# Kernel optimization log

Measured on AMD Instinct MI355X. Metric: run time of the kernel, lower is better.

The kernel has to match this reference:

```python
import jax, jax.numpy as jnp
import numpy as np

N = 100000        # nodes
E = 3200000       # edges (avg degree 32)
IN, HID, OUT = 512, 256, 64
K = 10
ALPHA = 0.1


def setup_inputs() -> dict:
    key = jax.random.key(0)
    k1, k2, k3, k4 = jax.random.split(key, 4)
    x = jax.random.normal(k1, (N, IN), dtype=jnp.float32)
    edge_index = jax.random.randint(k2, (2, E), 0, N, dtype=jnp.int64)
    W1 = jax.random.normal(k3, (IN, HID), dtype=jnp.float32) * (1.0 / np.sqrt(IN))
    b1 = jnp.zeros((HID,), dtype=jnp.float32)
    W2 = jax.random.normal(k4, (HID, OUT), dtype=jnp.float32) * (1.0 / np.sqrt(HID))
    b2 = jnp.zeros((OUT,), dtype=jnp.float32)
    return {"x": x, "edge_index": edge_index, "W1": W1, "b1": b1, "W2": W2, "b2": b2}


def reference(x, edge_index, W1, b1, W2, b2):
    # MLP head: Linear -> ReLU -> Linear
    h = jax.nn.relu(x @ W1 + b1)
    h = h @ W2 + b2                                   # [N, OUT]

    # gcn_norm with self-loops: D^-1/2 (A + I) D^-1/2
    src = jnp.concatenate([edge_index[0], jnp.arange(N, dtype=edge_index.dtype)])
    dst = jnp.concatenate([edge_index[1], jnp.arange(N, dtype=edge_index.dtype)])
    deg = jax.ops.segment_sum(jnp.ones_like(src, dtype=h.dtype), dst, num_segments=N)
    dinv = jnp.where(deg > 0, jax.lax.rsqrt(deg), 0.0)
    norm = dinv[src] * dinv[dst]                      # [E+N]

    h0 = h

    def step(h, _):
        msg = h[src] * norm[:, None]                  # gather + edge scale
        agg = jax.ops.segment_sum(msg, dst, num_segments=N)  # scatter-add
        h = (1.0 - ALPHA) * agg + ALPHA * h0          # teleport
        return h, None

    h, _ = jax.lax.scan(step, h, None, length=K)
    return h
```

## Files before the change

### kernel.cpp

```cpp
#include <hip/hip_runtime.h>
#include <hip/hip_bf16.h>
#include <hip/hip_fp16.h>


typedef __bf16 bf16x8 __attribute__((ext_vector_type(8)));
typedef float f32x4 __attribute__((ext_vector_type(4)));

static constexpr int IN = 512, HID = 256, OUT = 64;
static constexpr int LDT = 40;

static __device__ __forceinline__ ushort f2bf(float f) {
  __hip_bfloat16 b = __float2bfloat16(f);
  return *reinterpret_cast<ushort*>(&b);
}
static __device__ __forceinline__ float bf2f(ushort u) {
  unsigned int x = ((unsigned int)u) << 16;
  return __uint_as_float(x);
}
static __device__ __forceinline__ float h15f(unsigned int u) {
  ushort hb = (ushort)(u & 0x7FFFu);
  __half h = *reinterpret_cast<__half*>(&hb);
  return __half2float(h);
}

static __device__ __forceinline__ void gload16(const void* g, void* l) {
  __builtin_amdgcn_global_load_lds(
      (const __attribute__((address_space(1))) void*)g,
      (__attribute__((address_space(3))) void*)l, 16, 0, 0);
}

__global__ void transpose_f32_bf16(const float* __restrict__ in, ushort* __restrict__ out,
                                   int K, int C) {
  int idx = blockIdx.x * 256 + threadIdx.x;
  if (idx < K * C) {
    int n = idx / K, k = idx % K;
    out[idx] = f2bf(in[k * C + n]);
  }
}

__global__ __launch_bounds__(256) void gemm1(const float* __restrict__ X,
                                             const ushort* __restrict__ W1T,
                                             const float* __restrict__ b1,
                                             ushort* __restrict__ h1, int M) {
  __shared__ __align__(16) float As[2][128 * 32];
  __shared__ __align__(16) ushort Bs[2][128 * 32];
  const int tid = threadIdx.x;
  const int m0 = blockIdx.y * 128;
  const int n0 = blockIdx.x * 128;
  const int lane = tid & 63, w = tid >> 6;
  const int wr = w >> 1, wc = w & 1;
  const int lm = lane & 15, lq = lane >> 4;
  const int wbase = w * 64;

  auto STAGE = [&](int k0, int buf) {
#pragma unroll
    for (int i = 0; i < 4; ++i) {
      int idx = i * 256 + tid;
      int row = idx >> 3, ch = idx & 7;
      int gm = m0 + row; gm = gm < M ? gm : M - 1;
      int sch = ch ^ (row & 7);
      gload16(&X[(size_t)gm * IN + k0 + sch * 4], &As[buf][(i * 256 + wbase) * 4]);
    }
#pragma unroll
    for (int i = 0; i < 2; ++i) {
      int idx = i * 256 + tid;
      int row = idx >> 2, ch = idx & 3;
      int sch = ch ^ ((row ^ (row >> 2)) & 3);
      gload16(&W1T[(size_t)(n0 + row) * IN + k0 + sch * 8], &Bs[buf][(i * 256 + wbase) * 8]);
    }
  };

  f32x4 acc[4][4] = {};

  STAGE(0, 0);
  __syncthreads();

  int cur = 0;
  for (int k0 = 0; k0 < IN; k0 += 32) {
    if (k0 + 32 < IN) STAGE(k0 + 32, cur ^ 1);

    bf16x8 af[4], bq[4];
#pragma unroll
    for (int mi = 0; mi < 4; ++mi) {
      int r = wr * 64 + mi * 16 + lm;
      int k7 = r & 7;
      float4 x0 = *reinterpret_cast<const float4*>(&As[cur][r * 32 + ((2 * lq) ^ k7) * 4]);
      float4 x1 = *reinterpret_cast<const float4*>(&As[cur][r * 32 + ((2 * lq + 1) ^ k7) * 4]);
      union { ushort u[8]; bf16x8 v; } cv;
      cv.u[0] = f2bf(x0.x); cv.u[1] = f2bf(x0.y); cv.u[2] = f2bf(x0.z); cv.u[3] = f2bf(x0.w);
      cv.u[4] = f2bf(x1.x); cv.u[5] = f2bf(x1.y); cv.u[6] = f2bf(x1.z); cv.u[7] = f2bf(x1.w);
      af[mi] = cv.v;
    }
#pragma unroll
    for (int ni = 0; ni < 4; ++ni) {
      int r = wc * 64 + ni * 16 + lm;
      int key = (r ^ (r >> 2)) & 3;
      bq[ni] = *reinterpret_cast<const bf16x8*>(&Bs[cur][r * 32 + (lq ^ key) * 8]);
    }
#pragma unroll
    for (int mi = 0; mi < 4; ++mi)
#pragma unroll
      for (int ni = 0; ni < 4; ++ni)
        acc[mi][ni] = __builtin_amdgcn_mfma_f32_16x16x32_bf16(af[mi], bq[ni], acc[mi][ni], 0, 0, 0);

    __syncthreads();
    cur ^= 1;
  }

#pragma unroll
  for (int ni = 0; ni < 4; ++ni) {
    int col = n0 + wc * 64 + ni * 16 + lm;
    float bias = b1[col];
#pragma unroll
    for (int mi = 0; mi < 4; ++mi) {
#pragma unroll
      for (int rg = 0; rg < 4; ++rg) {
        int row = m0 + wr * 64 + mi * 16 + lq * 4 + rg;
        if (row < M) {
          float v = acc[mi][ni][rg] + bias;
          v = v > 0.f ? v : 0.f;
          h1[(size_t)row * HID + col] = f2bf(v);
        }
      }
    }
  }
}

__global__ __launch_bounds__(256) void gemm2(const ushort* __restrict__ h1,
                                             const ushort* __restrict__ W2T,
                                             const float* __restrict__ b2,
                                             float* __restrict__ H0f,
                                             ushort* __restrict__ H0b, int M) {
  __shared__ __align__(16) ushort As[128 * LDT];
  __shared__ __align__(16) ushort Bs[64 * LDT];
  const int tid = threadIdx.x;
  const int m0 = blockIdx.x * 128;
  const int lane = tid & 63, w = tid >> 6;
  const int lm = lane & 15, lq = lane >> 4;
  const int c = tid & 3, r = tid >> 2;

  f32x4 acc[2][4] = {};

  for (int k0 = 0; k0 < HID; k0 += 32) {
#pragma unroll
    for (int rr = 0; rr < 2; ++rr) {
      int m = r + rr * 64;
      int gm = m0 + m; gm = gm < M ? gm : M - 1;
      *reinterpret_cast<int4*>(&As[m * LDT + c * 8]) =
          *reinterpret_cast<const int4*>(&h1[(size_t)gm * HID + k0 + c * 8]);
    }
    *reinterpret_cast<int4*>(&Bs[r * LDT + c * 8]) =
        *reinterpret_cast<const int4*>(&W2T[(size_t)r * HID + k0 + c * 8]);
    __syncthreads();
    bf16x8 af[2], bq[4];
#pragma unroll
    for (int mi = 0; mi < 2; ++mi)
      af[mi] = *reinterpret_cast<const bf16x8*>(&As[(w * 32 + mi * 16 + lm) * LDT + lq * 8]);
#pragma unroll
    for (int ni = 0; ni < 4; ++ni)
      bq[ni] = *reinterpret_cast<const bf16x8*>(&Bs[(ni * 16 + lm) * LDT + lq * 8]);
#pragma unroll
    for (int mi = 0; mi < 2; ++mi)
#pragma unroll
      for (int ni = 0; ni < 4; ++ni)
        acc[mi][ni] = __builtin_amdgcn_mfma_f32_16x16x32_bf16(af[mi], bq[ni], acc[mi][ni], 0, 0, 0);
    __syncthreads();
  }

#pragma unroll
  for (int ni = 0; ni < 4; ++ni) {
    int col = ni * 16 + lm;
    float bias = b2[col];
#pragma unroll
    for (int mi = 0; mi < 2; ++mi) {
#pragma unroll
      for (int rg = 0; rg < 4; ++rg) {
        int row = m0 + w * 32 + mi * 16 + lq * 4 + rg;
        if (row < M) {
          float v = acc[mi][ni][rg] + bias;
          H0f[(size_t)row * OUT + col] = v;
          H0b[(size_t)row * OUT + col] = f2bf(v);
        }
      }
    }
  }
}

__global__ void count_deg(const int* __restrict__ ei, int* __restrict__ cnt, int E) {
  int e = blockIdx.x * 256 + threadIdx.x;
  if (e < E) atomicAdd(&cnt[ei[E + e]], 1);
}

__global__ void calc_dinv(const int* __restrict__ cnt, float* __restrict__ dinv, int n) {
  int v = blockIdx.x * 256 + threadIdx.x;
  if (v < n) dinv[v] = rsqrtf((float)cnt[v] + 1.0f);
}

__global__ __launch_bounds__(1024) void scan_p1(const int* __restrict__ cnt,
                                                int* __restrict__ bsum, int n) {
  __shared__ int wsum[16];
  const int tid = threadIdx.x, lane = tid & 63, wid = tid >> 6;
  int i0 = blockIdx.x * 4096 + tid * 4;
  int s = 0;
#pragma unroll
  for (int j = 0; j < 4; ++j) s += (i0 + j < n) ? cnt[i0 + j] : 0;
#pragma unroll
  for (int d = 1; d < 64; d <<= 1) s += __shfl_xor(s, d, 64);
  if (lane == 0) wsum[wid] = s;
  __syncthreads();
  if (tid == 0) {
    int t = 0;
#pragma unroll
    for (int i = 0; i < 16; ++i) t += wsum[i];
    bsum[blockIdx.x] = t;
  }
}

__global__ __launch_bounds__(1024) void scan_p2(int* __restrict__ bsum, int nb) {
  __shared__ int wsum[16];
  __shared__ int woff[16];
  const int tid = threadIdx.x, lane = tid & 63, wid = tid >> 6;
  int x = (tid < nb) ? bsum[tid] : 0;
  int val = x;
#pragma unroll
  for (int d = 1; d < 64; d <<= 1) {
    int t = __shfl_up(val, d, 64);
    if (lane >= d) val += t;
  }
  if (lane == 63) wsum[wid] = val;
  __syncthreads();
  if (wid == 0) {
    int s = (lane < 16) ? wsum[lane] : 0;
    int sv = s;
#pragma unroll
    for (int d = 1; d < 16; d <<= 1) {
      int t = __shfl_up(sv, d, 64);
      if (lane >= d) sv += t;
    }
    if (lane < 16) woff[lane] = sv - s;
  }
  __syncthreads();
  if (tid < nb) bsum[tid] = woff[wid] + (val - x);
}

__global__ __launch_bounds__(1024) void scan_p3(const int* __restrict__ cnt,
                                                const int* __restrict__ bsum,
                                                int* __restrict__ offs,
                                                int* __restrict__ cursor, int n) {
  __shared__ int wsum[16];
  __shared__ int woff[16];
  const int tid = threadIdx.x, lane = tid & 63, wid = tid >> 6;
  int i0 = blockIdx.x * 4096 + tid * 4;
  int x[4];
#pragma unroll
  for (int j = 0; j < 4; ++j) x[j] = (i0 + j < n) ? cnt[i0 + j] : 0;
  int tsum = x[0] + x[1] + x[2] + x[3];
  int val = tsum;
#pragma unroll
  for (int d = 1; d < 64; d <<= 1) {
    int t = __shfl_up(val, d, 64);
    if (lane >= d) val += t;
  }
  if (lane == 63) wsum[wid] = val;
  __syncthreads();
  if (wid == 0) {
    int s = (lane < 16) ? wsum[lane] : 0;
    int sv = s;
#pragma unroll
    for (int d = 1; d < 16; d <<= 1) {
      int t = __shfl_up(sv, d, 64);
      if (lane >= d) sv += t;
    }
    if (lane < 16) woff[lane] = sv - s;
  }
  __syncthreads();
  int excl = bsum[blockIdx.x] + woff[wid] + (val - tsum);
#pragma unroll
  for (int j = 0; j < 4; ++j) {
    if (i0 + j < n) { offs[i0 + j] = excl; cursor[i0 + j] = excl; }
    excl += x[j];
  }
  if (i0 < n && i0 + 4 >= n) offs[n] = excl;
}

__global__ void fill_csr(const int* __restrict__ ei, int* __restrict__ cursor,
                         const float* __restrict__ dinv, unsigned int* __restrict__ csr,
                         int E) {
  int e = blockIdx.x * 256 + threadIdx.x;
  if (e < E) {
    int s = ei[e], d = ei[E + e];
    int p = atomicAdd(&cursor[d], 1);
    float w = dinv[s] * dinv[d];
    __half hw = __float2half(w);
    unsigned int hb = *reinterpret_cast<ushort*>(&hw);
    csr[p] = (((unsigned int)s) << 15) | hb;
  }
}

template <bool FINAL>
__global__ __launch_bounds__(256) void prop_step(const ushort* __restrict__ hinb,
                                                 ushort* __restrict__ houtb,
                                                 float* __restrict__ out,
                                                 const float* __restrict__ h0,
                                                 const int* __restrict__ offs,
                                                 const unsigned int* __restrict__ csr,
                                                 const float* __restrict__ dinv, int n) {
  int gw = (blockIdx.x * 256 + threadIdx.x) >> 6;
  int lane = threadIdx.x & 63;
  if (gw >= n) return;
  const unsigned int* hin32 = (const unsigned int*)hinb;
  const int c = lane & 31;
  const int half = lane >> 5;
  float alo[8], ahi[8];
#pragma unroll
  for (int k = 0; k < 8; ++k) { alo[k] = 0.f; ahi[k] = 0.f; }
  int e0 = offs[gw], e1 = offs[gw + 1];
  for (int base = e0; base < e1; base += 64) {
    int rem = e1 - base;
    unsigned int my = (lane < rem) ? csr[base + lane] : 0u;
    int cnt = rem < 64 ? rem : 64;
    int cnt32 = (cnt + 31) & ~31;
    for (int j = 0; j < cnt32; j += 32) {
      unsigned int u[16];
#pragma unroll
      for (int k = 0; k < 16; ++k)
        u[k] = (unsigned int)__shfl((int)my, j + 2 * k + half);
      unsigned int v[16];
#pragma unroll
      for (int k = 0; k < 16; ++k)
        v[k] = hin32[(size_t)(u[k] >> 15) * 32 + c];
#pragma unroll
      for (int k = 0; k < 16; ++k) {
        float w = h15f(u[k]);
        float f0 = __uint_as_float(v[k] << 16);
        float f1 = __uint_as_float(v[k] & 0xFFFF0000u);
        alo[k & 7] = fmaf(w, f0, alo[k & 7]);
        ahi[k & 7] = fmaf(w, f1, ahi[k & 7]);
      }
    }
  }
  float a0 = ((alo[0] + alo[1]) + (alo[2] + alo[3])) + ((alo[4] + alo[5]) + (alo[6] + alo[7]));
  float a1 = ((ahi[0] + ahi[1]) + (ahi[2] + ahi[3])) + ((ahi[4] + ahi[5]) + (ahi[6] + ahi[7]));
  a0 += __shfl_xor(a0, 32, 64);
  a1 += __shfl_xor(a1, 32, 64);
  float dv = dinv[gw];
  unsigned int sv = hin32[(size_t)gw * 32 + c];
  float sx = __uint_as_float(sv << 16);
  float sy = __uint_as_float(sv & 0xFFFF0000u);
  float2 h0f = ((const float2*)h0)[(size_t)gw * 32 + c];
  float o0 = 0.9f * (a0 + dv * dv * sx) + 0.1f * h0f.x;
  float o1 = 0.9f * (a1 + dv * dv * sy) + 0.1f * h0f.y;
  if (FINAL) {
    if (half == 0) {
      float2 ov; ov.x = o0; ov.y = o1;
      ((float2*)out)[(size_t)gw * 32 + c] = ov;
    }
  } else {
    if (half == 1) {
      unsigned int pk = (unsigned int)f2bf(o0) | ((unsigned int)f2bf(o1) << 16);
      ((unsigned int*)houtb)[(size_t)gw * 32 + c] = pk;
    }
  }
}

extern "C" void kernel_launch(void* const* d_in, const int* in_sizes, int n_in,
                              void* d_out, int out_size, void* d_ws, size_t ws_size,
                              hipStream_t stream) {
  const float* X  = (const float*)d_in[0];
  const int*   EI = (const int*)d_in[1];
  const float* W1 = (const float*)d_in[2];
  const float* b1 = (const float*)d_in[3];
  const float* W2 = (const float*)d_in[4];
  const float* b2 = (const float*)d_in[5];
  float* out = (float*)d_out;

  const int N = in_sizes[0] / IN;
  const int E = in_sizes[1] / 2;

  char* ws = (char*)d_ws;
  size_t o = 0;
  auto alloc = [&](size_t b) {
    char* p = ws + o;
    o = (o + b + 255) & ~(size_t)255;
    return p;
  };
  float*  H0f  = (float*)alloc((size_t)N * OUT * 4);
  ushort* H0b  = (ushort*)alloc((size_t)N * OUT * 2);
  ushort* hAb  = (ushort*)alloc((size_t)N * OUT * 2);
  ushort* hBb  = (ushort*)alloc((size_t)N * OUT * 2);
  ushort* h1   = (ushort*)alloc((size_t)N * HID * 2);
  ushort* W1T  = (ushort*)alloc((size_t)IN * HID * 2);
  ushort* W2T  = (ushort*)alloc((size_t)HID * OUT * 2);
  int*    cnt  = (int*)alloc((size_t)N * 4);
  int*    offs = (int*)alloc((size_t)(N + 1) * 4);
  int*    curs = (int*)alloc((size_t)N * 4);
  int*    bsum = (int*)alloc((size_t)1024 * 4);
  float*  dinv = (float*)alloc((size_t)N * 4);
  unsigned int* csr = (unsigned int*)alloc((size_t)E * 4);
  (void)ws_size; (void)n_in; (void)out_size;

  transpose_f32_bf16<<<(IN * HID + 255) / 256, 256, 0, stream>>>(W1, W1T, IN, HID);
  transpose_f32_bf16<<<(HID * OUT + 255) / 256, 256, 0, stream>>>(W2, W2T, HID, OUT);

  gemm1<<<dim3(HID / 128, (N + 127) / 128), 256, 0, stream>>>(X, W1T, b1, h1, N);
  gemm2<<<(N + 127) / 128, 256, 0, stream>>>(h1, W2T, b2, H0f, H0b, N);

  hipMemsetAsync(cnt, 0, (size_t)N * 4, stream);
  count_deg<<<(E + 255) / 256, 256, 0, stream>>>(EI, cnt, E);
  calc_dinv<<<(N + 255) / 256, 256, 0, stream>>>(cnt, dinv, N);
  const int NB = (N + 4095) / 4096;
  scan_p1<<<NB, 1024, 0, stream>>>(cnt, bsum, N);
  scan_p2<<<1, 1024, 0, stream>>>(bsum, NB);
  scan_p3<<<NB, 1024, 0, stream>>>(cnt, bsum, offs, curs, N);
  fill_csr<<<(E + 255) / 256, 256, 0, stream>>>(EI, curs, dinv, csr, E);

  const int pgrid = (N * OUT + 255) / 256;
  prop_step<false><<<pgrid, 256, 0, stream>>>(H0b, hAb, nullptr, H0f, offs, csr, dinv, N);
  for (int i = 0; i < 4; ++i) {
    prop_step<false><<<pgrid, 256, 0, stream>>>(hAb, hBb, nullptr, H0f, offs, csr, dinv, N);
    prop_step<false><<<pgrid, 256, 0, stream>>>(hBb, hAb, nullptr, H0f, offs, csr, dinv, N);
  }
  prop_step<true><<<pgrid, 256, 0, stream>>>(hAb, nullptr, out, H0f, offs, csr, dinv, N);
}
```

Baseline: 1.223 ms.

## Build CSR via two-pass bucketed scatter with LDS atomics instead of global atomics

Replaces the per-edge global atomicAdd CSR fill with a two-level counting sort. Edges are first histogrammed and scattered into 512-node destination buckets using LDS counters, with a staging buffer that reuses the h1 activation memory. A second pass then places each edge within its bucket using LDS cursors. Because staging aliases h1, the GEMMs are moved after graph construction. The goal is to cut contended random global atomics and scattered writes, at the cost of extra kernel launches and roughly two more passes over edge data.

```diff
diff --git a/kernel.cpp b/kernel.cpp
--- a/kernel.cpp
+++ b/kernel.cpp
@@ -8,6 +8,8 @@
 
 static constexpr int IN = 512, HID = 256, OUT = 64;
 static constexpr int LDT = 40;
+static constexpr int CHB = 4096;
+static constexpr int BSH = 9;
 
 static __device__ __forceinline__ ushort f2bf(float f) {
   __hip_bfloat16 b = __float2bfloat16(f);
@@ -245,8 +247,7 @@
 
 __global__ __launch_bounds__(1024) void scan_p3(const int* __restrict__ cnt,
                                                 const int* __restrict__ bsum,
-                                                int* __restrict__ offs,
-                                                int* __restrict__ cursor, int n) {
+                                                int* __restrict__ offs, int n) {
   __shared__ int wsum[16];
   __shared__ int woff[16];
   const int tid = threadIdx.x, lane = tid & 63, wid = tid >> 6;
@@ -277,23 +278,64 @@
   int excl = bsum[blockIdx.x] + woff[wid] + (val - tsum);
 #pragma unroll
   for (int j = 0; j < 4; ++j) {
-    if (i0 + j < n) { offs[i0 + j] = excl; cursor[i0 + j] = excl; }
+    if (i0 + j < n) offs[i0 + j] = excl;
     excl += x[j];
   }
   if (i0 < n && i0 + 4 >= n) offs[n] = excl;
 }
 
-__global__ void fill_csr(const int* __restrict__ ei, int* __restrict__ cursor,
-                         const float* __restrict__ dinv, unsigned int* __restrict__ csr,
-                         int E) {
-  int e = blockIdx.x * 256 + threadIdx.x;
-  if (e < E) {
+__global__ __launch_bounds__(256) void hist_a(const int* __restrict__ ei,
+                                              int* __restrict__ mat, int E, int nblk) {
+  __shared__ int h[256];
+  h[threadIdx.x] = 0;
+  __syncthreads();
+  int e0 = blockIdx.x * CHB;
+  int e1 = e0 + CHB; if (e1 > E) e1 = E;
+  for (int e = e0 + threadIdx.x; e < e1; e += 256)
+    atomicAdd(&h[ei[E + e] >> BSH], 1);
+  __syncthreads();
+  mat[threadIdx.x * nblk + blockIdx.x] = h[threadIdx.x];
+}
+
+__global__ __launch_bounds__(256) void scatter_a(const int* __restrict__ ei,
+                                                 const int* __restrict__ mat,
+                                                 const float* __restrict__ dinv,
+                                                 uint2* __restrict__ stage,
+                                                 int E, int nblk) {
+  __shared__ int cur[256];
+  cur[threadIdx.x] = mat[threadIdx.x * nblk + blockIdx.x];
+  __syncthreads();
+  int e0 = blockIdx.x * CHB;
+  int e1 = e0 + CHB; if (e1 > E) e1 = E;
+  for (int e = e0 + threadIdx.x; e < e1; e += 256) {
     int s = ei[e], d = ei[E + e];
-    int p = atomicAdd(&cursor[d], 1);
     float w = dinv[s] * dinv[d];
     __half hw = __float2half(w);
     unsigned int hb = *reinterpret_cast<ushort*>(&hw);
-    csr[p] = (((unsigned int)s) << 15) | hb;
+    int p = atomicAdd(&cur[d >> BSH], 1);
+    uint2 r;
+    r.x = (((unsigned int)s) << 15) | hb;
+    r.y = (unsigned int)d;
+    stage[p] = r;
+  }
+}
+
+__global__ __launch_bounds__(256) void phase_b(const uint2* __restrict__ stage,
+                                               const int* __restrict__ offs,
+                                               unsigned int* __restrict__ csr, int n) {
+  __shared__ int lcur[1 << BSH];
+  const int n0 = blockIdx.x << BSH;
+  int n1 = n0 + (1 << BSH); if (n1 > n) n1 = n;
+  for (int t = threadIdx.x; t < (1 << BSH); t += 256) {
+    int node = n0 + t;
+    lcur[t] = (node < n) ? offs[node] : 0;
+  }
+  __syncthreads();
+  const int e0 = offs[n0], e1 = offs[n1];
+  for (int i = e0 + threadIdx.x; i < e1; i += 256) {
+    uint2 r = stage[i];
+    int p = atomicAdd(&lcur[r.y - (unsigned int)n0], 1);
+    csr[p] = r.x;
   }
 }
 
@@ -393,17 +435,17 @@
   ushort* W2T  = (ushort*)alloc((size_t)HID * OUT * 2);
   int*    cnt  = (int*)alloc((size_t)N * 4);
   int*    offs = (int*)alloc((size_t)(N + 1) * 4);
-  int*    curs = (int*)alloc((size_t)N * 4);
   int*    bsum = (int*)alloc((size_t)1024 * 4);
   float*  dinv = (float*)alloc((size_t)N * 4);
   unsigned int* csr = (unsigned int*)alloc((size_t)E * 4);
+  const int NBLK = (E + CHB - 1) / CHB;
+  int*    mat  = (int*)alloc((size_t)256 * NBLK * 4);
+  int*    msum = (int*)alloc((size_t)1024 * 4);
+  uint2*  stage = (uint2*)h1;
   (void)ws_size; (void)n_in; (void)out_size;
 
   transpose_f32_bf16<<<(IN * HID + 255) / 256, 256, 0, stream>>>(W1, W1T, IN, HID);
   transpose_f32_bf16<<<(HID * OUT + 255) / 256, 256, 0, stream>>>(W2, W2T, HID, OUT);
-
-  gemm1<<<dim3(HID / 128, (N + 127) / 128), 256, 0, stream>>>(X, W1T, b1, h1, N);
-  gemm2<<<(N + 127) / 128, 256, 0, stream>>>(h1, W2T, b2, H0f, H0b, N);
 
   hipMemsetAsync(cnt, 0, (size_t)N * 4, stream);
   count_deg<<<(E + 255) / 256, 256, 0, stream>>>(EI, cnt, E);
@@ -411,8 +453,20 @@
   const int NB = (N + 4095) / 4096;
   scan_p1<<<NB, 1024, 0, stream>>>(cnt, bsum, N);
   scan_p2<<<1, 1024, 0, stream>>>(bsum, NB);
-  scan_p3<<<NB, 1024, 0, stream>>>(cnt, bsum, offs, curs, N);
-  fill_csr<<<(E + 255) / 256, 256, 0, stream>>>(EI, curs, dinv, csr, E);
+  scan_p3<<<NB, 1024, 0, stream>>>(cnt, bsum, offs, N);
+
+  const int MN = 256 * NBLK;
+  const int MB = (MN + 4095) / 4096;
+  hist_a<<<NBLK, 256, 0, stream>>>(EI, mat, E, NBLK);
+  scan_p1<<<MB, 1024, 0, stream>>>(mat, msum, MN);
+  scan_p2<<<1, 1024, 0, stream>>>(msum, MB);
+  scan_p3<<<MB, 1024, 0, stream>>>(mat, msum, mat, MN);
+  scatter_a<<<NBLK, 256, 0, stream>>>(EI, mat, dinv, stage, E, NBLK);
+  const int NBKT = (N + (1 << BSH) - 1) >> BSH;
+  phase_b<<<NBKT, 256, 0, stream>>>(stage, offs, csr, N);
+
+  gemm1<<<dim3(HID / 128, (N + 127) / 128), 256, 0, stream>>>(X, W1T, b1, h1, N);
+  gemm2<<<(N + 127) / 128, 256, 0, stream>>>(h1, W2T, b2, H0f, H0b, N);
 
   const int pgrid = (N * OUT + 255) / 256;
   prop_step<false><<<pgrid, 256, 0, stream>>>(H0b, hAb, nullptr, H0f, offs, csr, dinv, N);
```

Result: no change. 1.201 ms (-1.8%).
